# Optimization experiments

Hardware: AMD Instinct MI355X
Metric: run time of the kernel (lower is better)

The kernel has to match this reference:

```python
import jax, jax.numpy as jnp
import numpy as np

B, N, D = 8, 4096, 6          # clouds, points per cloud, coordinate dim
K = 64                        # max_num_neighbors in radius query
NS1, NS2 = 2048, 512          # fps ratios 0.5 and 0.25
R1, R2 = 0.2, 0.4             # ball-query radii
DIMS = {1: [6, 64, 64, 128], 2: [134, 128, 128, 256], 3: [262, 256, 512, 1024], 4: [1024, 512, 512]}


def setup_inputs():
    key = jax.random.key(0)
    k0, k1, k2 = jax.random.split(key, 3)
    inp = {}
    inp['synapse_cordi'] = jax.random.normal(k0, (B * N, D), jnp.float32)
    inp['batch_index'] = jnp.repeat(jnp.arange(B, dtype=jnp.int32), N)
    inp['weight'] = jax.random.uniform(k1, (B * N,), jnp.float32)
    k = k2
    for i, dims in DIMS.items():
        for j in range(len(dims) - 1):
            k, kw = jax.random.split(k)
            inp[f'w{i}_{j}'] = jax.random.normal(kw, (dims[j], dims[j + 1]), jnp.float32) * (1.0 / float(np.sqrt(dims[j])))
            inp[f'b{i}_{j}'] = jnp.zeros((dims[j + 1],), jnp.float32)
    return inp


def _mlp(x, params):
    # PyG MLP, plain_last=True; batch-norm at default (eval, running stats) is identity
    n = len(params)
    for i, (W, b) in enumerate(params):
        x = x @ W + b
        if i < n - 1:
            x = jax.nn.relu(x)
    return x


def _fps(pos, n_s):
    # farthest point sampling on one cloud [N, D] -> [n_s] indices (deterministic start at 0)
    d0 = jnp.sum((pos - pos[0]) ** 2, axis=-1)
    def step(mind, _):
        nxt = jnp.argmax(mind)
        mind = jnp.minimum(mind, jnp.sum((pos - pos[nxt]) ** 2, axis=-1))
        return mind, nxt
    _, idxs = jax.lax.scan(step, d0, None, length=n_s - 1)
    return jnp.concatenate([jnp.zeros((1,), idxs.dtype), idxs])


def _ball(pos, pos_q, r):
    # radius query: up to K nearest points within r for each query; [n_q,K] idx + validity mask
    d2 = jnp.sum((pos_q[:, None, :] - pos[None, :, :]) ** 2, axis=-1)  # [n_q, N]
    neg = jnp.where(d2 <= r * r, -d2, -jnp.inf)
    vals, nbr = jax.lax.top_k(neg, K)
    return nbr, vals > -jnp.inf


def _sa(x, pos, params, n_s, r):
    # Weight_Sample_Module: fps -> radius -> PointNetConv (gather, MLP, masked max-scatter)
    idx = jax.vmap(lambda p: _fps(p, n_s))(pos)                     # [B, n_s]
    pos_q = jnp.take_along_axis(pos, idx[..., None], axis=1)        # [B, n_s, D]
    nbr, valid = jax.vmap(lambda p, q: _ball(p, q, r))(pos, pos_q)  # [B, n_s, K]
    gather = lambda a: jax.vmap(lambda t, i: t[i])(a, nbr)          # [B, n_s, K, C]
    rel = gather(pos) - pos_q[:, :, None, :]
    feat = rel if x is None else jnp.concatenate([gather(x), rel], axis=-1)
    h = _mlp(feat, params)                                          # [B, n_s, K, C_out]
    h = jnp.where(valid[..., None], h, -jnp.inf)
    return jnp.max(h, axis=2), pos_q                                # max aggregation


def reference(synapse_cordi, batch_index, weight,
              w1_0, b1_0, w1_1, b1_1, w1_2, b1_2,
              w2_0, b2_0, w2_1, b2_1, w2_2, b2_2,
              w3_0, b3_0, w3_1, b3_1, w3_2, b3_2,
              w4_0, b4_0, w4_1, b4_1):
    pos = synapse_cordi.reshape(B, N, D)  # uniform clouds; batch_index = repeat(arange(B), N)
    p1 = [(w1_0, b1_0), (w1_1, b1_1), (w1_2, b1_2)]
    p2 = [(w2_0, b2_0), (w2_1, b2_1), (w2_2, b2_2)]
    p3 = [(w3_0, b3_0), (w3_1, b3_1), (w3_2, b3_2)]
    p4 = [(w4_0, b4_0), (w4_1, b4_1)]
    x1, pos1 = _sa(None, pos, p1, NS1, R1)   # [B, 2048, 128]
    x2, pos2 = _sa(x1, pos1, p2, NS2, R2)    # [B, 512, 256]
    h = _mlp(jnp.concatenate([x2, pos2], axis=-1), p3)  # [B, 512, 1024]
    g = jnp.max(h, axis=1)                   # global max pool -> [B, 1024]
    return _mlp(g, p4)                       # [B, 512]
```

## Files before the change

kernel.cpp:

```cpp
#include <hip/hip_runtime.h>
#include <math.h>

#define B_ 8
#define N_ 4096
#define D_ 6
#define K_ 64
#define NS1_ 2048
#define NS2_ 512

typedef float v2f __attribute__((ext_vector_type(2)));


__device__ __forceinline__ float dist2_rn(const float* __restrict__ a, const float* __restrict__ q) {
    float s = 0.f;
#pragma unroll
    for (int d = 0; d < 6; ++d) {
        float diff = __fsub_rn(a[d], q[d]);
        s = __fadd_rn(s, __fmul_rn(diff, diff));
    }
    return s;
}

__device__ __forceinline__ unsigned mapf(float x) {
    unsigned u = __float_as_uint(x);
    return (u & 0x80000000u) ? ~u : (u | 0x80000000u);
}
__device__ __forceinline__ float unmapf(unsigned u) {
    return __uint_as_float((u & 0x80000000u) ? (u & 0x7FFFFFFFu) : ~u);
}

template <int CTRL>
__device__ __forceinline__ double dppd(double k) {
    int lo = __double2loint(k), hi = __double2hiint(k);
    int nlo = __builtin_amdgcn_update_dpp(lo, lo, CTRL, 0xF, 0xF, false);
    int nhi = __builtin_amdgcn_update_dpp(hi, hi, CTRL, 0xF, 0xF, false);
    return __hiloint2double(nhi, nlo);
}


__device__ __forceinline__ void wait_flag(unsigned* f, int t) {
    if (t == 0) {
        while (__hip_atomic_load(f, __ATOMIC_RELAXED, __HIP_MEMORY_SCOPE_AGENT) == 0u)
            __builtin_amdgcn_s_sleep(32);
        __builtin_amdgcn_fence(__ATOMIC_ACQUIRE, "agent");
    }
    __syncthreads();
}


template <int NP, int NS>
__device__ __forceinline__ void fps_core(float* __restrict__ spos, int* __restrict__ sidx,
                                         double* __restrict__ part, int t) {
#pragma clang fp contract(off)
    constexpr int NT = 256;
    constexpr int P = NP / NT;
    constexpr int HP = P / 2;
    int lane = t & 63, w = t >> 6;

    v2f px2[HP][6];
#pragma unroll
    for (int j = 0; j < HP; ++j)
#pragma unroll
        for (int d = 0; d < 6; ++d) {
            px2[j][d].x = spos[(t + NT * (2 * j)) * 6 + d];
            px2[j][d].y = spos[(t + NT * (2 * j + 1)) * 6 + d];
        }

    float cx[6];
#pragma unroll
    for (int d = 0; d < 6; ++d) cx[d] = spos[d];

    v2f mind2[HP];
    float runv = -1.f;
    int runj = 0;
#pragma unroll
    for (int j = 0; j < HP; ++j) {
        v2f d2 = {0.f, 0.f};
#pragma unroll
        for (int d = 0; d < 6; ++d) {
            v2f df = px2[j][d] - cx[d];
            d2 = d2 + df * df;
        }
        mind2[j] = d2;
        if (d2.x > runv) { runv = d2.x; runj = t + NT * (2 * j); }
        if (d2.y > runv) { runv = d2.y; runj = t + NT * (2 * j + 1); }
    }

    for (int s = 1; s < NS; ++s) {
        double key = __hiloint2double((int)__float_as_uint(runv), (int)(unsigned)(~runj));
        key = fmax(key, dppd<0x111>(key));
        key = fmax(key, dppd<0x112>(key));
        key = fmax(key, dppd<0x114>(key));
        key = fmax(key, dppd<0x118>(key));
        key = fmax(key, dppd<0x142>(key));
        key = fmax(key, dppd<0x143>(key));
        if (lane == 63) part[(s & 1) * 4 + w] = key;
        __syncthreads();
        double kk = part[(s & 1) * 4 + (lane & 3)];
        kk = fmax(kk, dppd<0x111>(kk));
        kk = fmax(kk, dppd<0x112>(kk));
        int nx = ~__builtin_amdgcn_readlane(__double2loint(kk), 3);
        if (t == 0) sidx[s] = nx;

        const float2* sv2 = (const float2*)spos;
        float2 ca = sv2[nx * 3], cb = sv2[nx * 3 + 1], cc = sv2[nx * 3 + 2];
        cx[0] = ca.x; cx[1] = ca.y; cx[2] = cb.x; cx[3] = cb.y; cx[4] = cc.x; cx[5] = cc.y;

        runv = -1.f;
        runj = 0;
#pragma unroll
        for (int j = 0; j < HP; ++j) {
            v2f d2 = {0.f, 0.f};
#pragma unroll
            for (int d = 0; d < 6; ++d) {
                v2f df = px2[j][d] - cx[d];
                d2 = d2 + df * df;
            }
            float mx = fminf(mind2[j].x, d2.x);
            float my = fminf(mind2[j].y, d2.y);
            mind2[j].x = mx;
            mind2[j].y = my;
            if (mx > runv) { runv = mx; runj = t + NT * (2 * j); }
            if (my > runv) { runv = my; runj = t + NT * (2 * j + 1); }
        }
    }
}


template <int NPTS, int S>
__device__ __forceinline__ void ball_scan(const float* __restrict__ sp,
                                          const float* __restrict__ posq,
                                          int* __restrict__ nbr, int* __restrict__ cnt,
                                          float r2, int qid, int tid,
                                          float* __restrict__ sd, unsigned short* __restrict__ si) {
    float q[6];
#pragma unroll
    for (int d = 0; d < 6; ++d) q[d] = posq[(size_t)qid * 6 + d];

    int n = 0;
    float thr = INFINITY;
#pragma unroll 4
    for (int j = 0; j < NPTS; ++j) {
        float d2 = dist2_rn(sp + j * 6, q);
        if (d2 <= r2 && (n < K_ || d2 < thr)) {
            int i = (n < K_) ? n : (K_ - 1);
            if (n < K_) ++n;
            while (i > 0 && sd[(i - 1) * S + tid] > d2) {
                sd[i * S + tid] = sd[(i - 1) * S + tid];
                si[i * S + tid] = si[(i - 1) * S + tid];
                --i;
            }
            sd[i * S + tid] = d2;
            si[i * S + tid] = (unsigned short)j;
            if (n == K_) thr = sd[(K_ - 1) * S + tid];
        }
    }
    cnt[qid] = n;
    for (int i = 0; i < n; ++i) nbr[(size_t)qid * K_ + i] = (int)si[i * S + tid];
}


__global__ __launch_bounds__(256, 1) void stage12_kernel(
        const float* __restrict__ pos, float* __restrict__ pos1,
        int* __restrict__ nbr1, int* __restrict__ cnt1,
        float* __restrict__ pos2, int* __restrict__ nbr2, int* __restrict__ cnt2,
        unsigned* __restrict__ g, unsigned* flags,
        float r2_1, float r2_2) {
    __shared__ union Smem {
        struct { float spos[N_ * 6]; int sidx[NS1_]; double part[8]; } fps;
        struct { float spos[N_ * 6]; float sd[K_ * 128]; unsigned short si[K_ * 128]; } b1;
        struct { float spos[NS1_ * 6]; float sd[K_ * 64]; unsigned short si[K_ * 64]; } b2;
    } sm;
    int t = threadIdx.x;

    if (blockIdx.x < 8) {
        int b = blockIdx.x;
        float* spos = sm.fps.spos;
        int* sidx = sm.fps.sidx;
        double* part = sm.fps.part;

        {
            const float4* src = (const float4*)(pos + (size_t)b * N_ * 6);
            float4* dst = (float4*)spos;
            for (int e = t; e < N_ * 6 / 4; e += 256) dst[e] = src[e];
        }
        if (t == 0) sidx[0] = 0;
        __syncthreads();

        fps_core<N_, NS1_>(spos, sidx, part, t);
        __syncthreads();

        float smp[NS1_ / 256][6];
#pragma unroll
        for (int i = 0; i < NS1_ / 256; ++i) {
            int s = t + 256 * i;
            int ix = sidx[s];
#pragma unroll
            for (int d = 0; d < 6; ++d) smp[i][d] = spos[ix * 6 + d];
        }
#pragma unroll
        for (int i = 0; i < NS1_ / 256; ++i) {
            int s = t + 256 * i;
#pragma unroll
            for (int d = 0; d < 6; ++d) pos1[((size_t)b * NS1_ + s) * 6 + d] = smp[i][d];
        }
        __syncthreads();
        if (t == 0) {
            __threadfence();
            __hip_atomic_store(&flags[b], 1u, __ATOMIC_RELEASE, __HIP_MEMORY_SCOPE_AGENT);
        }

#pragma unroll
        for (int i = 0; i < NS1_ / 256; ++i) {
            int s = t + 256 * i;
#pragma unroll
            for (int d = 0; d < 6; ++d) spos[s * 6 + d] = smp[i][d];
        }
        for (int e = t; e < 1024; e += 256) g[b * 1024 + e] = 0u;
        if (t == 0) sidx[0] = 0;
        __syncthreads();

        fps_core<NS1_, NS2_>(spos, sidx, part, t);
        __syncthreads();

        for (int s = t; s < NS2_; s += 256) {
            int ix = sidx[s];
#pragma unroll
            for (int d = 0; d < 6; ++d) pos2[((size_t)b * NS2_ + s) * 6 + d] = spos[ix * 6 + d];
        }
        __syncthreads();
        if (t == 0) {
            __threadfence();
            __hip_atomic_store(&flags[8 + b], 1u, __ATOMIC_RELEASE, __HIP_MEMORY_SCOPE_AGENT);
        }
    } else if (blockIdx.x < 8 + 128) {
        int blk = blockIdx.x - 8;
        int b = blk >> 4;
        {
            const float4* src = (const float4*)(pos + (size_t)b * N_ * 6);
            float4* dst = (float4*)sm.b1.spos;
            for (int e = t; e < N_ * 6 / 4; e += 256) dst[e] = src[e];
        }
        __syncthreads();
        wait_flag(&flags[b], t);
        if (t < 128) {
            int qid = blk * 128 + t;
            ball_scan<N_, 128>(sm.b1.spos, pos1, nbr1, cnt1, r2_1, qid, t, sm.b1.sd, sm.b1.si);
        }
    } else {
        int blk = blockIdx.x - 136;
        int b = blk >> 3;
        wait_flag(&flags[b], t);
        {
            const float4* src = (const float4*)(pos1 + (size_t)b * NS1_ * 6);
            float4* dst = (float4*)sm.b2.spos;
            for (int e = t; e < NS1_ * 6 / 4; e += 256) dst[e] = src[e];
        }
        __syncthreads();
        wait_flag(&flags[8 + b], t);
        if (t < 64) {
            int qid = blk * 64 + t;
            ball_scan<NS1_, 64>(sm.b2.spos, pos2, nbr2, cnt2, r2_2, qid, t, sm.b2.sd, sm.b2.si);
        }
    }
}


__global__ __launch_bounds__(256) void sa1_kernel(const float* __restrict__ pos,
                                                  const float* __restrict__ pos1,
                                                  const int* __restrict__ nbr1,
                                                  const int* __restrict__ cnt1,
                                                  const float* __restrict__ W1, const float* __restrict__ B1,
                                                  const float* __restrict__ W2, const float* __restrict__ B2,
                                                  const float* __restrict__ W3, const float* __restrict__ B3,
                                                  float* __restrict__ x1) {
    int lane = threadIdx.x & 63;
    int w = threadIdx.x >> 6;
    int qid = blockIdx.x * 4 + w;
    int b = qid / NS1_;
    const float* p = pos + (size_t)b * N_ * 6;
    float q[6];
#pragma unroll
    for (int d = 0; d < 6; ++d) q[d] = pos1[(size_t)qid * 6 + d];
    int c = cnt1[qid];
    float m0 = -INFINITY, m1 = -INFINITY;

    for (int n = 0; n < c; ++n) {
        int j = nbr1[(size_t)qid * K_ + n];
        float rel[6];
#pragma unroll
        for (int d = 0; d < 6; ++d) rel[d] = p[(size_t)j * 6 + d] - q[d];
        float a = B1[lane];
#pragma unroll
        for (int d = 0; d < 6; ++d) a = fmaf(W1[d * 64 + lane], rel[d], a);
        float h1 = fmaxf(a, 0.f);
        float a2 = B2[lane];
        for (int k = 0; k < 64; ++k) {
            float v = __shfl(h1, k, 64);
            a2 = fmaf(W2[k * 64 + lane], v, a2);
        }
        float h2 = fmaxf(a2, 0.f);
        float o0 = B3[lane], o1 = B3[64 + lane];
        for (int k = 0; k < 64; ++k) {
            float v = __shfl(h2, k, 64);
            o0 = fmaf(W3[k * 128 + lane], v, o0);
            o1 = fmaf(W3[k * 128 + 64 + lane], v, o1);
        }
        m0 = fmaxf(m0, o0);
        m1 = fmaxf(m1, o1);
    }
    x1[(size_t)qid * 128 + lane] = m0;
    x1[(size_t)qid * 128 + 64 + lane] = m1;
}


__global__ __launch_bounds__(256) void sa2_conv(const float* __restrict__ pos1, const float* __restrict__ posq,
                                                const int* __restrict__ nbr, const int* __restrict__ cnt,
                                                const float* __restrict__ x1,
                                                const float* __restrict__ W1, const float* __restrict__ B1,
                                                const float* __restrict__ W2, const float* __restrict__ B2,
                                                const float* __restrict__ W3, const float* __restrict__ B3,
                                                float* __restrict__ out) {
    int lane = threadIdx.x & 63;
    int w = threadIdx.x >> 6;
    int qid = blockIdx.x * 4 + w;
    int b = qid / NS2_;
    float q[6];
#pragma unroll
    for (int d = 0; d < 6; ++d) q[d] = posq[(size_t)qid * 6 + d];
    int c = cnt[qid];
    float m0 = -INFINITY, m1 = -INFINITY, m2 = -INFINITY, m3 = -INFINITY;

    for (int n = 0; n < c; ++n) {
        int j = nbr[(size_t)qid * K_ + n];
        size_t row = (size_t)b * NS1_ + j;
        const float* xs = x1 + row * 128;
        float rel[6];
#pragma unroll
        for (int d = 0; d < 6; ++d) rel[d] = pos1[row * 6 + d] - q[d];
        float a0 = B1[lane], a1 = B1[64 + lane];
        for (int k = 0; k < 128; ++k) {
            float v = xs[k];
            a0 = fmaf(W1[k * 128 + lane], v, a0);
            a1 = fmaf(W1[k * 128 + 64 + lane], v, a1);
        }
#pragma unroll
        for (int d = 0; d < 6; ++d) {
            float v = rel[d];
            a0 = fmaf(W1[(128 + d) * 128 + lane], v, a0);
            a1 = fmaf(W1[(128 + d) * 128 + 64 + lane], v, a1);
        }
        float h1a = fmaxf(a0, 0.f), h1b = fmaxf(a1, 0.f);
        float c0 = B2[lane], c1 = B2[64 + lane];
        for (int k = 0; k < 64; ++k) {
            float v = __shfl(h1a, k, 64);
            c0 = fmaf(W2[k * 128 + lane], v, c0);
            c1 = fmaf(W2[k * 128 + 64 + lane], v, c1);
        }
        for (int k = 0; k < 64; ++k) {
            float v = __shfl(h1b, k, 64);
            c0 = fmaf(W2[(64 + k) * 128 + lane], v, c0);
            c1 = fmaf(W2[(64 + k) * 128 + 64 + lane], v, c1);
        }
        float h2a = fmaxf(c0, 0.f), h2b = fmaxf(c1, 0.f);
        float e0 = B3[lane], e1 = B3[64 + lane], e2 = B3[128 + lane], e3 = B3[192 + lane];
        for (int k = 0; k < 64; ++k) {
            float v = __shfl(h2a, k, 64);
            e0 = fmaf(W3[k * 256 + lane], v, e0);
            e1 = fmaf(W3[k * 256 + 64 + lane], v, e1);
            e2 = fmaf(W3[k * 256 + 128 + lane], v, e2);
            e3 = fmaf(W3[k * 256 + 192 + lane], v, e3);
        }
        for (int k = 0; k < 64; ++k) {
            float v = __shfl(h2b, k, 64);
            e0 = fmaf(W3[(64 + k) * 256 + lane], v, e0);
            e1 = fmaf(W3[(64 + k) * 256 + 64 + lane], v, e1);
            e2 = fmaf(W3[(64 + k) * 256 + 128 + lane], v, e2);
            e3 = fmaf(W3[(64 + k) * 256 + 192 + lane], v, e3);
        }
        m0 = fmaxf(m0, e0);
        m1 = fmaxf(m1, e1);
        m2 = fmaxf(m2, e2);
        m3 = fmaxf(m3, e3);
    }
    out[(size_t)qid * 256 + lane] = m0;
    out[(size_t)qid * 256 + 64 + lane] = m1;
    out[(size_t)qid * 256 + 128 + lane] = m2;
    out[(size_t)qid * 256 + 192 + lane] = m3;
}


__global__ __launch_bounds__(256, 1) void mlp3_kernel(const float* __restrict__ x2, const float* __restrict__ pos2,
                                                      const float* __restrict__ W0, const float* __restrict__ B0,
                                                      const float* __restrict__ W1, const float* __restrict__ B1,
                                                      const float* __restrict__ W2, const float* __restrict__ B2,
                                                      unsigned* __restrict__ g) {
    int lane = threadIdx.x & 63;
    int w = threadIdx.x >> 6;
    int qid0 = blockIdx.x * 16 + w * 4;
    int b = qid0 >> 9;

    float xr[4][4];
#pragma unroll
    for (int q = 0; q < 4; ++q)
#pragma unroll
        for (int j = 0; j < 4; ++j) xr[q][j] = x2[(size_t)(qid0 + q) * 256 + j * 64 + lane];

    float a[4][4];
    {
        float4 bv = *(const float4*)&B0[lane * 4];
#pragma unroll
        for (int q = 0; q < 4; ++q) { a[q][0] = bv.x; a[q][1] = bv.y; a[q][2] = bv.z; a[q][3] = bv.w; }
    }
#pragma unroll
    for (int j = 0; j < 4; ++j) {
        for (int k2 = 0; k2 < 64; ++k2) {
            int k = j * 64 + k2;
            float4 wv = *(const float4*)&W0[(size_t)k * 256 + lane * 4];
#pragma unroll
            for (int q = 0; q < 4; ++q) {
                float v = __shfl(xr[q][j], k2, 64);
                a[q][0] = fmaf(wv.x, v, a[q][0]);
                a[q][1] = fmaf(wv.y, v, a[q][1]);
                a[q][2] = fmaf(wv.z, v, a[q][2]);
                a[q][3] = fmaf(wv.w, v, a[q][3]);
            }
        }
    }
#pragma unroll
    for (int d = 0; d < 6; ++d) {
        float4 wv = *(const float4*)&W0[(size_t)(256 + d) * 256 + lane * 4];
#pragma unroll
        for (int q = 0; q < 4; ++q) {
            float v = pos2[(size_t)(qid0 + q) * 6 + d];
            a[q][0] = fmaf(wv.x, v, a[q][0]);
            a[q][1] = fmaf(wv.y, v, a[q][1]);
            a[q][2] = fmaf(wv.z, v, a[q][2]);
            a[q][3] = fmaf(wv.w, v, a[q][3]);
        }
    }
    float h1[4][4];
#pragma unroll
    for (int q = 0; q < 4; ++q)
#pragma unroll
        for (int u = 0; u < 4; ++u) h1[q][u] = fmaxf(a[q][u], 0.f);

    float c[4][8];
    {
        float4 b0 = *(const float4*)&B1[lane * 8];
        float4 b1 = *(const float4*)&B1[lane * 8 + 4];
#pragma unroll
        for (int q = 0; q < 4; ++q) {
            c[q][0] = b0.x; c[q][1] = b0.y; c[q][2] = b0.z; c[q][3] = b0.w;
            c[q][4] = b1.x; c[q][5] = b1.y; c[q][6] = b1.z; c[q][7] = b1.w;
        }
    }
    for (int l = 0; l < 64; ++l) {
#pragma unroll
        for (int r = 0; r < 4; ++r) {
            int k = l * 4 + r;
            float4 w0 = *(const float4*)&W1[(size_t)k * 512 + lane * 8];
            float4 w1 = *(const float4*)&W1[(size_t)k * 512 + lane * 8 + 4];
#pragma unroll
            for (int q = 0; q < 4; ++q) {
                float v = __shfl(h1[q][r], l, 64);
                c[q][0] = fmaf(w0.x, v, c[q][0]);
                c[q][1] = fmaf(w0.y, v, c[q][1]);
                c[q][2] = fmaf(w0.z, v, c[q][2]);
                c[q][3] = fmaf(w0.w, v, c[q][3]);
                c[q][4] = fmaf(w1.x, v, c[q][4]);
                c[q][5] = fmaf(w1.y, v, c[q][5]);
                c[q][6] = fmaf(w1.z, v, c[q][6]);
                c[q][7] = fmaf(w1.w, v, c[q][7]);
            }
        }
    }
    float h2[4][8];
#pragma unroll
    for (int q = 0; q < 4; ++q)
#pragma unroll
        for (int u = 0; u < 8; ++u) h2[q][u] = fmaxf(c[q][u], 0.f);

    float e[4][16];
#pragma unroll
    for (int jj = 0; jj < 4; ++jj) {
        float4 bv = *(const float4*)&B2[lane * 16 + jj * 4];
#pragma unroll
        for (int q = 0; q < 4; ++q) {
            e[q][jj * 4 + 0] = bv.x; e[q][jj * 4 + 1] = bv.y;
            e[q][jj * 4 + 2] = bv.z; e[q][jj * 4 + 3] = bv.w;
        }
    }
    for (int l = 0; l < 64; ++l) {
#pragma unroll
        for (int r = 0; r < 8; ++r) {
            int k = l * 8 + r;
            const float* wp = &W2[(size_t)k * 1024 + lane * 16];
            float4 w0 = *(const float4*)&wp[0];
            float4 w1 = *(const float4*)&wp[4];
            float4 w2 = *(const float4*)&wp[8];
            float4 w3 = *(const float4*)&wp[12];
#pragma unroll
            for (int q = 0; q < 4; ++q) {
                float v = __shfl(h2[q][r], l, 64);
                e[q][0]  = fmaf(w0.x, v, e[q][0]);
                e[q][1]  = fmaf(w0.y, v, e[q][1]);
                e[q][2]  = fmaf(w0.z, v, e[q][2]);
                e[q][3]  = fmaf(w0.w, v, e[q][3]);
                e[q][4]  = fmaf(w1.x, v, e[q][4]);
                e[q][5]  = fmaf(w1.y, v, e[q][5]);
                e[q][6]  = fmaf(w1.z, v, e[q][6]);
                e[q][7]  = fmaf(w1.w, v, e[q][7]);
                e[q][8]  = fmaf(w2.x, v, e[q][8]);
                e[q][9]  = fmaf(w2.y, v, e[q][9]);
                e[q][10] = fmaf(w2.z, v, e[q][10]);
                e[q][11] = fmaf(w2.w, v, e[q][11]);
                e[q][12] = fmaf(w3.x, v, e[q][12]);
                e[q][13] = fmaf(w3.y, v, e[q][13]);
                e[q][14] = fmaf(w3.z, v, e[q][14]);
                e[q][15] = fmaf(w3.w, v, e[q][15]);
            }
        }
    }
#pragma unroll
    for (int u = 0; u < 16; ++u) {
        float m = fmaxf(fmaxf(e[0][u], e[1][u]), fmaxf(e[2][u], e[3][u]));
        atomicMax(&g[b * 1024 + lane * 16 + u], mapf(m));
    }
}


__global__ __launch_bounds__(512) void mlp4_kernel(const unsigned* __restrict__ g,
                                                   const float* __restrict__ W0, const float* __restrict__ B0,
                                                   const float* __restrict__ W1, const float* __restrict__ B1,
                                                   float* __restrict__ out) {
    int b = blockIdx.x;
    int c = threadIdx.x;
    __shared__ float h[512];
    float a = B0[c];
    for (int k = 0; k < 1024; ++k) {
        float v = unmapf(g[b * 1024 + k]);
        a = fmaf(v, W0[k * 512 + c], a);
    }
    h[c] = fmaxf(a, 0.f);
    __syncthreads();
    float o = B1[c];
    for (int k = 0; k < 512; ++k) o = fmaf(h[k], W1[k * 512 + c], o);
    out[(size_t)b * 512 + c] = o;
}


extern "C" void kernel_launch(void* const* d_in, const int* in_sizes, int n_in,
                              void* d_out, int out_size, void* d_ws, size_t ws_size,
                              hipStream_t stream) {
    const float* pos = (const float*)d_in[0];
    const float* w1_0 = (const float*)d_in[3];
    const float* b1_0 = (const float*)d_in[4];
    const float* w1_1 = (const float*)d_in[5];
    const float* b1_1 = (const float*)d_in[6];
    const float* w1_2 = (const float*)d_in[7];
    const float* b1_2 = (const float*)d_in[8];
    const float* w2_0 = (const float*)d_in[9];
    const float* b2_0 = (const float*)d_in[10];
    const float* w2_1 = (const float*)d_in[11];
    const float* b2_1 = (const float*)d_in[12];
    const float* w2_2 = (const float*)d_in[13];
    const float* b2_2 = (const float*)d_in[14];
    const float* w3_0 = (const float*)d_in[15];
    const float* b3_0 = (const float*)d_in[16];
    const float* w3_1 = (const float*)d_in[17];
    const float* b3_1 = (const float*)d_in[18];
    const float* w3_2 = (const float*)d_in[19];
    const float* b3_2 = (const float*)d_in[20];
    const float* w4_0 = (const float*)d_in[21];
    const float* b4_0 = (const float*)d_in[22];
    const float* w4_1 = (const float*)d_in[23];
    const float* b4_1 = (const float*)d_in[24];
    float* out = (float*)d_out;

    char* ws = (char*)d_ws;
    size_t off = 0;
    float* pos1 = (float*)(ws + off);  off += (size_t)B_ * NS1_ * 6 * 4;
    int* nbr1 = (int*)(ws + off);      off += (size_t)B_ * NS1_ * K_ * 4;
    int* cnt1 = (int*)(ws + off);      off += (size_t)B_ * NS1_ * 4;
    float* x1 = (float*)(ws + off);    off += (size_t)B_ * NS1_ * 128 * 4;
    float* pos2 = (float*)(ws + off);  off += (size_t)B_ * NS2_ * 6 * 4;
    int* nbr2 = (int*)(ws + off);      off += (size_t)B_ * NS2_ * K_ * 4;
    int* cnt2 = (int*)(ws + off);      off += (size_t)B_ * NS2_ * 4;
    float* x2 = (float*)(ws + off);    off += (size_t)B_ * NS2_ * 256 * 4;
    unsigned* g = (unsigned*)(ws + off); off += (size_t)B_ * 1024 * 4;
    unsigned* flags = (unsigned*)(ws + off); off += 64;

    const float r2_1 = (float)(0.2 * 0.2);
    const float r2_2 = (float)(0.4 * 0.4);

    hipMemsetAsync(flags, 0, 64, stream);

    stage12_kernel<<<200, 256, 0, stream>>>(pos, pos1, nbr1, cnt1, pos2, nbr2, cnt2, g,
                                            flags, r2_1, r2_2);
    sa1_kernel<<<(B_ * NS1_) / 4, 256, 0, stream>>>(pos, pos1, nbr1, cnt1,
                                                    w1_0, b1_0, w1_1, b1_1, w1_2, b1_2, x1);
    sa2_conv<<<(B_ * NS2_) / 4, 256, 0, stream>>>(pos1, pos2, nbr2, cnt2, x1,
                                                  w2_0, b2_0, w2_1, b2_1, w2_2, b2_2, x2);
    mlp3_kernel<<<(B_ * NS2_) / 16, 256, 0, stream>>>(x2, pos2, w3_0, b3_0, w3_1, b3_1, w3_2, b3_2, g);
    mlp4_kernel<<<B_, 512, 0, stream>>>(g, w4_0, b4_0, w4_1, b4_1, out);
}
```

Before: 2.497 ms.

## Fuse ball query, SA1/SA2 convs and MLP3 into one persistent kernel

Folds the SA1 conv, SA2 conv and MLP3 global max-pool into the stage12 kernel. Each of 128 worker blocks runs its ball query and then immediately applies the MLP using the neighbor lists and point positions already in shared memory, so the nbr/cnt/x2 arrays are never written to global memory. A per-batch counter flag is added so SA2 can wait until every SA1 block of its cloud has finished, and the separate sa1/sa2/mlp3 launches are removed. The cost is that all the heavy MLP work now runs on only 128 blocks of 4 waves. That is far less parallelism than the thousands of blocks the separate kernels used, and the extra spin-waits can serialize further.

After: 2.770 ms. 10.9% more time.

```diff
diff --git a/kernel.cpp b/kernel.cpp
--- a/kernel.cpp
+++ b/kernel.cpp
@@ -42,6 +42,15 @@
     if (t == 0) {
         while (__hip_atomic_load(f, __ATOMIC_RELAXED, __HIP_MEMORY_SCOPE_AGENT) == 0u)
             __builtin_amdgcn_s_sleep(32);
+        __builtin_amdgcn_fence(__ATOMIC_ACQUIRE, "agent");
+    }
+    __syncthreads();
+}
+
+__device__ __forceinline__ void wait_count(unsigned* f, unsigned tgt, int t) {
+    if (t == 0) {
+        while (__hip_atomic_load(f, __ATOMIC_RELAXED, __HIP_MEMORY_SCOPE_AGENT) < tgt)
+            __builtin_amdgcn_s_sleep(8);
         __builtin_amdgcn_fence(__ATOMIC_ACQUIRE, "agent");
     }
     __syncthreads();
@@ -128,11 +137,10 @@
 
 
 template <int NPTS, int S>
-__device__ __forceinline__ void ball_scan(const float* __restrict__ sp,
-                                          const float* __restrict__ posq,
-                                          int* __restrict__ nbr, int* __restrict__ cnt,
-                                          float r2, int qid, int tid,
-                                          float* __restrict__ sd, unsigned short* __restrict__ si) {
+__device__ __forceinline__ int ball_scan(const float* __restrict__ sp,
+                                         const float* __restrict__ posq,
+                                         float r2, int qid, int tid,
+                                         float* __restrict__ sd, unsigned short* __restrict__ si) {
     float q[6];
 #pragma unroll
     for (int d = 0; d < 6; ++d) q[d] = posq[(size_t)qid * 6 + d];
@@ -155,23 +163,32 @@
             if (n == K_) thr = sd[(K_ - 1) * S + tid];
         }
     }
-    cnt[qid] = n;
-    for (int i = 0; i < n; ++i) nbr[(size_t)qid * K_ + i] = (int)si[i * S + tid];
+    return n;
 }
 
 
 __global__ __launch_bounds__(256, 1) void stage12_kernel(
-        const float* __restrict__ pos, float* __restrict__ pos1,
-        int* __restrict__ nbr1, int* __restrict__ cnt1,
-        float* __restrict__ pos2, int* __restrict__ nbr2, int* __restrict__ cnt2,
-        unsigned* __restrict__ g, unsigned* flags,
+        const float* __restrict__ pos, float* __restrict__ pos1, float* __restrict__ pos2,
+        float* __restrict__ x1, unsigned* __restrict__ g, unsigned* flags,
+        const float* __restrict__ W1_0, const float* __restrict__ B1_0,
+        const float* __restrict__ W1_1, const float* __restrict__ B1_1,
+        const float* __restrict__ W1_2, const float* __restrict__ B1_2,
+        const float* __restrict__ W2_0, const float* __restrict__ B2_0,
+        const float* __restrict__ W2_1, const float* __restrict__ B2_1,
+        const float* __restrict__ W2_2, const float* __restrict__ B2_2,
+        const float* __restrict__ W3_0, const float* __restrict__ B3_0,
+        const float* __restrict__ W3_1, const float* __restrict__ B3_1,
+        const float* __restrict__ W3_2, const float* __restrict__ B3_2,
         float r2_1, float r2_2) {
     __shared__ union Smem {
         struct { float spos[N_ * 6]; int sidx[NS1_]; double part[8]; } fps;
-        struct { float spos[N_ * 6]; float sd[K_ * 128]; unsigned short si[K_ * 128]; } b1;
-        struct { float spos[NS1_ * 6]; float sd[K_ * 64]; unsigned short si[K_ * 64]; } b2;
+        struct { float spos[N_ * 6]; float sd[K_ * 128]; unsigned short si[K_ * 128];
+                 unsigned short scnt[128]; } p1;
+        struct { float spos1[NS1_ * 6]; float sd2[K_ * 32]; unsigned short si2[K_ * 32];
+                 unsigned short scnt2[32]; float sx2[32 * 256]; } p2;
     } sm;
     int t = threadIdx.x;
+    int lane = t & 63, w = t >> 6;
 
     if (blockIdx.x < 8) {
         int b = blockIdx.x;
@@ -233,299 +250,281 @@
             __threadfence();
             __hip_atomic_store(&flags[8 + b], 1u, __ATOMIC_RELEASE, __HIP_MEMORY_SCOPE_AGENT);
         }
-    } else if (blockIdx.x < 8 + 128) {
-        int blk = blockIdx.x - 8;
-        int b = blk >> 4;
+        return;
+    }
+
+    int blk = blockIdx.x - 8;
+    int b = blk >> 4, sub = blk & 15;
+
+    {
+        const float4* src = (const float4*)(pos + (size_t)b * N_ * 6);
+        float4* dst = (float4*)sm.p1.spos;
+        for (int e = t; e < N_ * 6 / 4; e += 256) dst[e] = src[e];
+    }
+    __syncthreads();
+    wait_flag(&flags[b], t);
+
+    int qbase1 = b * NS1_ + sub * 128;
+    if (t < 128) {
+        int n = ball_scan<N_, 128>(sm.p1.spos, pos1, r2_1, qbase1 + t, t, sm.p1.sd, sm.p1.si);
+        sm.p1.scnt[t] = (unsigned short)n;
+    }
+    __syncthreads();
+
+    for (int qq = 0; qq < 32; ++qq) {
+        int lq = w * 32 + qq;
+        int qid = qbase1 + lq;
+        float q[6];
+#pragma unroll
+        for (int d = 0; d < 6; ++d) q[d] = pos1[(size_t)qid * 6 + d];
+        int c = sm.p1.scnt[lq];
+        float m0 = -INFINITY, m1 = -INFINITY;
+        for (int n = 0; n < c; ++n) {
+            int j = sm.p1.si[n * 128 + lq];
+            float rel[6];
+#pragma unroll
+            for (int d = 0; d < 6; ++d) rel[d] = sm.p1.spos[j * 6 + d] - q[d];
+            float a = B1_0[lane];
+#pragma unroll
+            for (int d = 0; d < 6; ++d) a = fmaf(W1_0[d * 64 + lane], rel[d], a);
+            float h1 = fmaxf(a, 0.f);
+            float a2 = B1_1[lane];
+            for (int k = 0; k < 64; ++k) {
+                float v = __shfl(h1, k, 64);
+                a2 = fmaf(W1_1[k * 64 + lane], v, a2);
+            }
+            float h2 = fmaxf(a2, 0.f);
+            float o0 = B1_2[lane], o1 = B1_2[64 + lane];
+            for (int k = 0; k < 64; ++k) {
+                float v = __shfl(h2, k, 64);
+                o0 = fmaf(W1_2[k * 128 + lane], v, o0);
+                o1 = fmaf(W1_2[k * 128 + 64 + lane], v, o1);
+            }
+            m0 = fmaxf(m0, o0);
+            m1 = fmaxf(m1, o1);
+        }
+        x1[(size_t)qid * 128 + lane] = m0;
+        x1[(size_t)qid * 128 + 64 + lane] = m1;
+    }
+    __syncthreads();
+    if (t == 0) {
+        __threadfence();
+        __hip_atomic_fetch_add(&flags[16 + b], 1u, __ATOMIC_RELEASE, __HIP_MEMORY_SCOPE_AGENT);
+    }
+
+    {
+        const float4* src = (const float4*)(pos1 + (size_t)b * NS1_ * 6);
+        float4* dst = (float4*)sm.p2.spos1;
+        for (int e = t; e < NS1_ * 6 / 4; e += 256) dst[e] = src[e];
+    }
+    __syncthreads();
+    wait_flag(&flags[8 + b], t);
+
+    int qbase2 = b * NS2_ + sub * 32;
+    if (t < 32) {
+        int n = ball_scan<NS1_, 32>(sm.p2.spos1, pos2, r2_2, qbase2 + t, t, sm.p2.sd2, sm.p2.si2);
+        sm.p2.scnt2[t] = (unsigned short)n;
+    }
+    __syncthreads();
+    wait_count(&flags[16 + b], 16u, t);
+
+    for (int qq = 0; qq < 8; ++qq) {
+        int lq = w * 8 + qq;
+        int qid = qbase2 + lq;
+        float q[6];
+#pragma unroll
+        for (int d = 0; d < 6; ++d) q[d] = pos2[(size_t)qid * 6 + d];
+        int c = sm.p2.scnt2[lq];
+        float m0 = -INFINITY, m1 = -INFINITY, m2 = -INFINITY, m3 = -INFINITY;
+        for (int n = 0; n < c; ++n) {
+            int j = sm.p2.si2[n * 32 + lq];
+            const float* xs = x1 + ((size_t)b * NS1_ + j) * 128;
+            float rel[6];
+#pragma unroll
+            for (int d = 0; d < 6; ++d) rel[d] = sm.p2.spos1[j * 6 + d] - q[d];
+            float a0 = B2_0[lane], a1 = B2_0[64 + lane];
+            for (int k = 0; k < 128; ++k) {
+                float v = xs[k];
+                a0 = fmaf(W2_0[k * 128 + lane], v, a0);
+                a1 = fmaf(W2_0[k * 128 + 64 + lane], v, a1);
+            }
+#pragma unroll
+            for (int d = 0; d < 6; ++d) {
+                float v = rel[d];
+                a0 = fmaf(W2_0[(128 + d) * 128 + lane], v, a0);
+                a1 = fmaf(W2_0[(128 + d) * 128 + 64 + lane], v, a1);
+            }
+            float h1a = fmaxf(a0, 0.f), h1b = fmaxf(a1, 0.f);
+            float c0 = B2_1[lane], c1 = B2_1[64 + lane];
+            for (int k = 0; k < 64; ++k) {
+                float v = __shfl(h1a, k, 64);
+                c0 = fmaf(W2_1[k * 128 + lane], v, c0);
+                c1 = fmaf(W2_1[k * 128 + 64 + lane], v, c1);
+            }
+            for (int k = 0; k < 64; ++k) {
+                float v = __shfl(h1b, k, 64);
+                c0 = fmaf(W2_1[(64 + k) * 128 + lane], v, c0);
+                c1 = fmaf(W2_1[(64 + k) * 128 + 64 + lane], v, c1);
+            }
+            float h2a = fmaxf(c0, 0.f), h2b = fmaxf(c1, 0.f);
+            float e0 = B2_2[lane], e1 = B2_2[64 + lane], e2 = B2_2[128 + lane], e3 = B2_2[192 + lane];
+            for (int k = 0; k < 64; ++k) {
+                float v = __shfl(h2a, k, 64);
+                e0 = fmaf(W2_2[k * 256 + lane], v, e0);
+                e1 = fmaf(W2_2[k * 256 + 64 + lane], v, e1);
+                e2 = fmaf(W2_2[k * 256 + 128 + lane], v, e2);
+                e3 = fmaf(W2_2[k * 256 + 192 + lane], v, e3);
+            }
+            for (int k = 0; k < 64; ++k) {
+                float v = __shfl(h2b, k, 64);
+                e0 = fmaf(W2_2[(64 + k) * 256 + lane], v, e0);
+                e1 = fmaf(W2_2[(64 + k) * 256 + 64 + lane], v, e1);
+                e2 = fmaf(W2_2[(64 + k) * 256 + 128 + lane], v, e2);
+                e3 = fmaf(W2_2[(64 + k) * 256 + 192 + lane], v, e3);
+            }
+            m0 = fmaxf(m0, e0);
+            m1 = fmaxf(m1, e1);
+            m2 = fmaxf(m2, e2);
+            m3 = fmaxf(m3, e3);
+        }
+        sm.p2.sx2[lq * 256 + lane] = m0;
+        sm.p2.sx2[lq * 256 + 64 + lane] = m1;
+        sm.p2.sx2[lq * 256 + 128 + lane] = m2;
+        sm.p2.sx2[lq * 256 + 192 + lane] = m3;
+    }
+    __syncthreads();
+
+    for (int pass = 0; pass < 2; ++pass) {
+        int lq0 = w * 8 + pass * 4;
+        int qid0 = qbase2 + lq0;
+
+        float xr[4][4];
+#pragma unroll
+        for (int q = 0; q < 4; ++q)
+#pragma unroll
+            for (int j = 0; j < 4; ++j) xr[q][j] = sm.p2.sx2[(lq0 + q) * 256 + j * 64 + lane];
+
+        float a[4][4];
         {
-            const float4* src = (const float4*)(pos + (size_t)b * N_ * 6);
-            float4* dst = (float4*)sm.b1.spos;
-            for (int e = t; e < N_ * 6 / 4; e += 256) dst[e] = src[e];
-        }
-        __syncthreads();
-        wait_flag(&flags[b], t);
-        if (t < 128) {
-            int qid = blk * 128 + t;
-            ball_scan<N_, 128>(sm.b1.spos, pos1, nbr1, cnt1, r2_1, qid, t, sm.b1.sd, sm.b1.si);
-        }
-    } else {
-        int blk = blockIdx.x - 136;
-        int b = blk >> 3;
-        wait_flag(&flags[b], t);
-        {
-            const float4* src = (const float4*)(pos1 + (size_t)b * NS1_ * 6);
-            float4* dst = (float4*)sm.b2.spos;
-            for (int e = t; e < NS1_ * 6 / 4; e += 256) dst[e] = src[e];
-        }
-        __syncthreads();
-        wait_flag(&flags[8 + b], t);
-        if (t < 64) {
-            int qid = blk * 64 + t;
-            ball_scan<NS1_, 64>(sm.b2.spos, pos2, nbr2, cnt2, r2_2, qid, t, sm.b2.sd, sm.b2.si);
-        }
-    }
-}
-
-
-__global__ __launch_bounds__(256) void sa1_kernel(const float* __restrict__ pos,
-                                                  const float* __restrict__ pos1,
-                                                  const int* __restrict__ nbr1,
-                                                  const int* __restrict__ cnt1,
-                                                  const float* __restrict__ W1, const float* __restrict__ B1,
-                                                  const float* __restrict__ W2, const float* __restrict__ B2,
-                                                  const float* __restrict__ W3, const float* __restrict__ B3,
-                                                  float* __restrict__ x1) {
-    int lane = threadIdx.x & 63;
-    int w = threadIdx.x >> 6;
-    int qid = blockIdx.x * 4 + w;
-    int b = qid / NS1_;
-    const float* p = pos + (size_t)b * N_ * 6;
-    float q[6];
-#pragma unroll
-    for (int d = 0; d < 6; ++d) q[d] = pos1[(size_t)qid * 6 + d];
-    int c = cnt1[qid];
-    float m0 = -INFINITY, m1 = -INFINITY;
-
-    for (int n = 0; n < c; ++n) {
-        int j = nbr1[(size_t)qid * K_ + n];
-        float rel[6];
-#pragma unroll
-        for (int d = 0; d < 6; ++d) rel[d] = p[(size_t)j * 6 + d] - q[d];
-        float a = B1[lane];
-#pragma unroll
-        for (int d = 0; d < 6; ++d) a = fmaf(W1[d * 64 + lane], rel[d], a);
-        float h1 = fmaxf(a, 0.f);
-        float a2 = B2[lane];
-        for (int k = 0; k < 64; ++k) {
-            float v = __shfl(h1, k, 64);
-            a2 = fmaf(W2[k * 64 + lane], v, a2);
-        }
-        float h2 = fmaxf(a2, 0.f);
-        float o0 = B3[lane], o1 = B3[64 + lane];
-        for (int k = 0; k < 64; ++k) {
-            float v = __shfl(h2, k, 64);
-            o0 = fmaf(W3[k * 128 + lane], v, o0);
-            o1 = fmaf(W3[k * 128 + 64 + lane], v, o1);
-        }
-        m0 = fmaxf(m0, o0);
-        m1 = fmaxf(m1, o1);
-    }
-    x1[(size_t)qid * 128 + lane] = m0;
-    x1[(size_t)qid * 128 + 64 + lane] = m1;
-}
-
-
-__global__ __launch_bounds__(256) void sa2_conv(const float* __restrict__ pos1, const float* __restrict__ posq,
-                                                const int* __restrict__ nbr, const int* __restrict__ cnt,
-                                                const float* __restrict__ x1,
-                                                const float* __restrict__ W1, const float* __restrict__ B1,
-                                                const float* __restrict__ W2, const float* __restrict__ B2,
-                                                const float* __restrict__ W3, const float* __restrict__ B3,
-                                                float* __restrict__ out) {
-    int lane = threadIdx.x & 63;
-    int w = threadIdx.x >> 6;
-    int qid = blockIdx.x * 4 + w;
-    int b = qid / NS2_;
-    float q[6];
-#pragma unroll
-    for (int d = 0; d < 6; ++d) q[d] = posq[(size_t)qid * 6 + d];
-    int c = cnt[qid];
-    float m0 = -INFINITY, m1 = -INFINITY, m2 = -INFINITY, m3 = -INFINITY;
-
-    for (int n = 0; n < c; ++n) {
-        int j = nbr[(size_t)qid * K_ + n];
-        size_t row = (size_t)b * NS1_ + j;
-        const float* xs = x1 + row * 128;
-        float rel[6];
-#pragma unroll
-        for (int d = 0; d < 6; ++d) rel[d] = pos1[row * 6 + d] - q[d];
-        float a0 = B1[lane], a1 = B1[64 + lane];
-        for (int k = 0; k < 128; ++k) {
-            float v = xs[k];
-            a0 = fmaf(W1[k * 128 + lane], v, a0);
-            a1 = fmaf(W1[k * 128 + 64 + lane], v, a1);
+            float4 bv = *(const float4*)&B3_0[lane * 4];
+#pragma unroll
+            for (int q = 0; q < 4; ++q) { a[q][0] = bv.x; a[q][1] = bv.y; a[q][2] = bv.z; a[q][3] = bv.w; }
+        }
+#pragma unroll
+        for (int j = 0; j < 4; ++j) {
+            for (int k2 = 0; k2 < 64; ++k2) {
+                int k = j * 64 + k2;
+                float4 wv = *(const float4*)&W3_0[(size_t)k * 256 + lane * 4];
+#pragma unroll
+                for (int q = 0; q < 4; ++q) {
+                    float v = __shfl(xr[q][j], k2, 64);
+                    a[q][0] = fmaf(wv.x, v, a[q][0]);
+                    a[q][1] = fmaf(wv.y, v, a[q][1]);
+                    a[q][2] = fmaf(wv.z, v, a[q][2]);
+                    a[q][3] = fmaf(wv.w, v, a[q][3]);
+                }
+            }
         }
 #pragma unroll
         for (int d = 0; d < 6; ++d) {
-            float v = rel[d];
-            a0 = fmaf(W1[(128 + d) * 128 + lane], v, a0);
-            a1 = fmaf(W1[(128 + d) * 128 + 64 + lane], v, a1);
-        }
-        float h1a = fmaxf(a0, 0.f), h1b = fmaxf(a1, 0.f);
-        float c0 = B2[lane], c1 = B2[64 + lane];
-        for (int k = 0; k < 64; ++k) {
-            float v = __shfl(h1a, k, 64);
-            c0 = fmaf(W2[k * 128 + lane], v, c0);
-            c1 = fmaf(W2[k * 128 + 64 + lane], v, c1);
-        }
-        for (int k = 0; k < 64; ++k) {
-            float v = __shfl(h1b, k, 64);
-            c0 = fmaf(W2[(64 + k) * 128 + lane], v, c0);
-            c1 = fmaf(W2[(64 + k) * 128 + 64 + lane], v, c1);
-        }
-        float h2a = fmaxf(c0, 0.f), h2b = fmaxf(c1, 0.f);
-        float e0 = B3[lane], e1 = B3[64 + lane], e2 = B3[128 + lane], e3 = B3[192 + lane];
-        for (int k = 0; k < 64; ++k) {
-            float v = __shfl(h2a, k, 64);
-            e0 = fmaf(W3[k * 256 + lane], v, e0);
-            e1 = fmaf(W3[k * 256 + 64 + lane], v, e1);
-            e2 = fmaf(W3[k * 256 + 128 + lane], v, e2);
-            e3 = fmaf(W3[k * 256 + 192 + lane], v, e3);
-        }
-        for (int k = 0; k < 64; ++k) {
-            float v = __shfl(h2b, k, 64);
-            e0 = fmaf(W3[(64 + k) * 256 + lane], v, e0);
-            e1 = fmaf(W3[(64 + k) * 256 + 64 + lane], v, e1);
-            e2 = fmaf(W3[(64 + k) * 256 + 128 + lane], v, e2);
-            e3 = fmaf(W3[(64 + k) * 256 + 192 + lane], v, e3);
-        }
-        m0 = fmaxf(m0, e0);
-        m1 = fmaxf(m1, e1);
-        m2 = fmaxf(m2, e2);
-        m3 = fmaxf(m3, e3);
-    }
-    out[(size_t)qid * 256 + lane] = m0;
-    out[(size_t)qid * 256 + 64 + lane] = m1;
-    out[(size_t)qid * 256 + 128 + lane] = m2;
-    out[(size_t)qid * 256 + 192 + lane] = m3;
-}
-
-
-__global__ __launch_bounds__(256, 1) void mlp3_kernel(const float* __restrict__ x2, const float* __restrict__ pos2,
-                                                      const float* __restrict__ W0, const float* __restrict__ B0,
-                                                      const float* __restrict__ W1, const float* __restrict__ B1,
-                                                      const float* __restrict__ W2, const float* __restrict__ B2,
-                                                      unsigned* __restrict__ g) {
-    int lane = threadIdx.x & 63;
-    int w = threadIdx.x >> 6;
-    int qid0 = blockIdx.x * 16 + w * 4;
-    int b = qid0 >> 9;
-
-    float xr[4][4];
-#pragma unroll
-    for (int q = 0; q < 4; ++q)
-#pragma unroll
-        for (int j = 0; j < 4; ++j) xr[q][j] = x2[(size_t)(qid0 + q) * 256 + j * 64 + lane];
-
-    float a[4][4];
-    {
-        float4 bv = *(const float4*)&B0[lane * 4];
-#pragma unroll
-        for (int q = 0; q < 4; ++q) { a[q][0] = bv.x; a[q][1] = bv.y; a[q][2] = bv.z; a[q][3] = bv.w; }
-    }
-#pragma unroll
-    for (int j = 0; j < 4; ++j) {
-        for (int k2 = 0; k2 < 64; ++k2) {
-            int k = j * 64 + k2;
-            float4 wv = *(const float4*)&W0[(size_t)k * 256 + lane * 4];
+            float4 wv = *(const float4*)&W3_0[(size_t)(256 + d) * 256 + lane * 4];
 #pragma unroll
             for (int q = 0; q < 4; ++q) {
-                float v = __shfl(xr[q][j], k2, 64);
+                float v = pos2[(size_t)(qid0 + q) * 6 + d];
                 a[q][0] = fmaf(wv.x, v, a[q][0]);
                 a[q][1] = fmaf(wv.y, v, a[q][1]);
                 a[q][2] = fmaf(wv.z, v, a[q][2]);
                 a[q][3] = fmaf(wv.w, v, a[q][3]);
             }
         }
-    }
-#pragma unroll
-    for (int d = 0; d < 6; ++d) {
-        float4 wv = *(const float4*)&W0[(size_t)(256 + d) * 256 + lane * 4];
-#pragma unroll
-        for (int q = 0; q < 4; ++q) {
-            float v = pos2[(size_t)(qid0 + q) * 6 + d];
-            a[q][0] = fmaf(wv.x, v, a[q][0]);
-            a[q][1] = fmaf(wv.y, v, a[q][1]);
-            a[q][2] = fmaf(wv.z, v, a[q][2]);
-            a[q][3] = fmaf(wv.w, v, a[q][3]);
-        }
-    }
-    float h1[4][4];
-#pragma unroll
-    for (int q = 0; q < 4; ++q)
-#pragma unroll
-        for (int u = 0; u < 4; ++u) h1[q][u] = fmaxf(a[q][u], 0.f);
-
-    float c[4][8];
-    {
-        float4 b0 = *(const float4*)&B1[lane * 8];
-        float4 b1 = *(const float4*)&B1[lane * 8 + 4];
-#pragma unroll
-        for (int q = 0; q < 4; ++q) {
-            c[q][0] = b0.x; c[q][1] = b0.y; c[q][2] = b0.z; c[q][3] = b0.w;
-            c[q][4] = b1.x; c[q][5] = b1.y; c[q][6] = b1.z; c[q][7] = b1.w;
-        }
-    }
-    for (int l = 0; l < 64; ++l) {
-#pragma unroll
-        for (int r = 0; r < 4; ++r) {
-            int k = l * 4 + r;
-            float4 w0 = *(const float4*)&W1[(size_t)k * 512 + lane * 8];
-            float4 w1 = *(const float4*)&W1[(size_t)k * 512 + lane * 8 + 4];
+        float h1[4][4];
+#pragma unroll
+        for (int q = 0; q < 4; ++q)
+#pragma unroll
+            for (int u = 0; u < 4; ++u) h1[q][u] = fmaxf(a[q][u], 0.f);
+
+        float c[4][8];
+        {
+            float4 b0 = *(const float4*)&B3_1[lane * 8];
+            float4 b1 = *(const float4*)&B3_1[lane * 8 + 4];
 #pragma unroll
             for (int q = 0; q < 4; ++q) {
-                float v = __shfl(h1[q][r], l, 64);
-                c[q][0] = fmaf(w0.x, v, c[q][0]);
-                c[q][1] = fmaf(w0.y, v, c[q][1]);
-                c[q][2] = fmaf(w0.z, v, c[q][2]);
-                c[q][3] = fmaf(w0.w, v, c[q][3]);
-                c[q][4] = fmaf(w1.x, v, c[q][4]);
-                c[q][5] = fmaf(w1.y, v, c[q][5]);
-                c[q][6] = fmaf(w1.z, v, c[q][6]);
-                c[q][7] = fmaf(w1.w, v, c[q][7]);
-            }
-        }
-    }
-    float h2[4][8];
-#pragma unroll
-    for (int q = 0; q < 4; ++q)
-#pragma unroll
-        for (int u = 0; u < 8; ++u) h2[q][u] = fmaxf(c[q][u], 0.f);
-
-    float e[4][16];
-#pragma unroll
-    for (int jj = 0; jj < 4; ++jj) {
-        float4 bv = *(const float4*)&B2[lane * 16 + jj * 4];
-#pragma unroll
-        for (int q = 0; q < 4; ++q) {
-            e[q][jj * 4 + 0] = bv.x; e[q][jj * 4 + 1] = bv.y;
-            e[q][jj * 4 + 2] = bv.z; e[q][jj * 4 + 3] = bv.w;
-        }
-    }
-    for (int l = 0; l < 64; ++l) {
-#pragma unroll
-        for (int r = 0; r < 8; ++r) {
-            int k = l * 8 + r;
-            const float* wp = &W2[(size_t)k * 1024 + lane * 16];
-            float4 w0 = *(const float4*)&wp[0];
-            float4 w1 = *(const float4*)&wp[4];
-            float4 w2 = *(const float4*)&wp[8];
-            float4 w3 = *(const float4*)&wp[12];
+                c[q][0] = b0.x; c[q][1] = b0.y; c[q][2] = b0.z; c[q][3] = b0.w;
+                c[q][4] = b1.x; c[q][5] = b1.y; c[q][6] = b1.z; c[q][7] = b1.w;
+            }
+        }
+        for (int l = 0; l < 64; ++l) {
+#pragma unroll
+            for (int r = 0; r < 4; ++r) {
+                int k = l * 4 + r;
+                float4 w0 = *(const float4*)&W3_1[(size_t)k * 512 + lane * 8];
+                float4 w1 = *(const float4*)&W3_1[(size_t)k * 512 + lane * 8 + 4];
+#pragma unroll
+                for (int q = 0; q < 4; ++q) {
+                    float v = __shfl(h1[q][r], l, 64);
+                    c[q][0] = fmaf(w0.x, v, c[q][0]);
+                    c[q][1] = fmaf(w0.y, v, c[q][1]);
+                    c[q][2] = fmaf(w0.z, v, c[q][2]);
+                    c[q][3] = fmaf(w0.w, v, c[q][3]);
+                    c[q][4] = fmaf(w1.x, v, c[q][4]);
+                    c[q][5] = fmaf(w1.y, v, c[q][5]);
+                    c[q][6] = fmaf(w1.z, v, c[q][6]);
+                    c[q][7] = fmaf(w1.w, v, c[q][7]);
+                }
+            }
+        }
+        float h2[4][8];
+#pragma unroll
+        for (int q = 0; q < 4; ++q)
+#pragma unroll
+            for (int u = 0; u < 8; ++u) h2[q][u] = fmaxf(c[q][u], 0.f);
+
+        float e[4][16];
+#pragma unroll
+        for (int jj = 0; jj < 4; ++jj) {
+            float4 bv = *(const float4*)&B3_2[lane * 16 + jj * 4];
 #pragma unroll
             for (int q = 0; q < 4; ++q) {
-                float v = __shfl(h2[q][r], l, 64);
-                e[q][0]  = fmaf(w0.x, v, e[q][0]);
-                e[q][1]  = fmaf(w0.y, v, e[q][1]);
-                e[q][2]  = fmaf(w0.z, v, e[q][2]);
-                e[q][3]  = fmaf(w0.w, v, e[q][3]);
-                e[q][4]  = fmaf(w1.x, v, e[q][4]);
-                e[q][5]  = fmaf(w1.y, v, e[q][5]);
-                e[q][6]  = fmaf(w1.z, v, e[q][6]);
-                e[q][7]  = fmaf(w1.w, v, e[q][7]);
-                e[q][8]  = fmaf(w2.x, v, e[q][8]);
-                e[q][9]  = fmaf(w2.y, v, e[q][9]);
-                e[q][10] = fmaf(w2.z, v, e[q][10]);
-                e[q][11] = fmaf(w2.w, v, e[q][11]);
-                e[q][12] = fmaf(w3.x, v, e[q][12]);
-                e[q][13] = fmaf(w3.y, v, e[q][13]);
-                e[q][14] = fmaf(w3.z, v, e[q][14]);
-                e[q][15] = fmaf(w3.w, v, e[q][15]);
-            }
-        }
-    }
-#pragma unroll
-    for (int u = 0; u < 16; ++u) {
-        float m = fmaxf(fmaxf(e[0][u], e[1][u]), fmaxf(e[2][u], e[3][u]));
-        atomicMax(&g[b * 1024 + lane * 16 + u], mapf(m));
+                e[q][jj * 4 + 0] = bv.x; e[q][jj * 4 + 1] = bv.y;
+                e[q][jj * 4 + 2] = bv.z; e[q][jj * 4 + 3] = bv.w;
+            }
+        }
+        for (int l = 0; l < 64; ++l) {
+#pragma unroll
+            for (int r = 0; r < 8; ++r) {
+                int k = l * 8 + r;
+                const float* wp = &W3_2[(size_t)k * 1024 + lane * 16];
+                float4 w0 = *(const float4*)&wp[0];
+                float4 w1 = *(const float4*)&wp[4];
+                float4 w2 = *(const float4*)&wp[8];
+                float4 w3 = *(const float4*)&wp[12];
+#pragma unroll
+                for (int q = 0; q < 4; ++q) {
+                    float v = __shfl(h2[q][r], l, 64);
+                    e[q][0]  = fmaf(w0.x, v, e[q][0]);
+                    e[q][1]  = fmaf(w0.y, v, e[q][1]);
+                    e[q][2]  = fmaf(w0.z, v, e[q][2]);
+                    e[q][3]  = fmaf(w0.w, v, e[q][3]);
+                    e[q][4]  = fmaf(w1.x, v, e[q][4]);
+                    e[q][5]  = fmaf(w1.y, v, e[q][5]);
+                    e[q][6]  = fmaf(w1.z, v, e[q][6]);
+                    e[q][7]  = fmaf(w1.w, v, e[q][7]);
+                    e[q][8]  = fmaf(w2.x, v, e[q][8]);
+                    e[q][9]  = fmaf(w2.y, v, e[q][9]);
+                    e[q][10] = fmaf(w2.z, v, e[q][10]);
+                    e[q][11] = fmaf(w2.w, v, e[q][11]);
+                    e[q][12] = fmaf(w3.x, v, e[q][12]);
+                    e[q][13] = fmaf(w3.y, v, e[q][13]);
+                    e[q][14] = fmaf(w3.z, v, e[q][14]);
+                    e[q][15] = fmaf(w3.w, v, e[q][15]);
+                }
+            }
+        }
+#pragma unroll
+        for (int u = 0; u < 16; ++u) {
+            float m = fmaxf(fmaxf(e[0][u], e[1][u]), fmaxf(e[2][u], e[3][u]));
+            atomicMax(&g[b * 1024 + lane * 16 + u], mapf(m));
+        }
     }
 }
 
@@ -580,28 +579,21 @@
 
     char* ws = (char*)d_ws;
     size_t off = 0;
-    float* pos1 = (float*)(ws + off);  off += (size_t)B_ * NS1_ * 6 * 4;
-    int* nbr1 = (int*)(ws + off);      off += (size_t)B_ * NS1_ * K_ * 4;
-    int* cnt1 = (int*)(ws + off);      off += (size_t)B_ * NS1_ * 4;
-    float* x1 = (float*)(ws + off);    off += (size_t)B_ * NS1_ * 128 * 4;
-    float* pos2 = (float*)(ws + off);  off += (size_t)B_ * NS2_ * 6 * 4;
-    int* nbr2 = (int*)(ws + off);      off += (size_t)B_ * NS2_ * K_ * 4;
-    int* cnt2 = (int*)(ws + off);      off += (size_t)B_ * NS2_ * 4;
-    float* x2 = (float*)(ws + off);    off += (size_t)B_ * NS2_ * 256 * 4;
+    float* pos1 = (float*)(ws + off);    off += (size_t)B_ * NS1_ * 6 * 4;
+    float* pos2 = (float*)(ws + off);    off += (size_t)B_ * NS2_ * 6 * 4;
+    float* x1 = (float*)(ws + off);      off += (size_t)B_ * NS1_ * 128 * 4;
     unsigned* g = (unsigned*)(ws + off); off += (size_t)B_ * 1024 * 4;
-    unsigned* flags = (unsigned*)(ws + off); off += 64;
+    unsigned* flags = (unsigned*)(ws + off); off += 32 * 4;
 
     const float r2_1 = (float)(0.2 * 0.2);
     const float r2_2 = (float)(0.4 * 0.4);
 
-    hipMemsetAsync(flags, 0, 64, stream);
-
-    stage12_kernel<<<200, 256, 0, stream>>>(pos, pos1, nbr1, cnt1, pos2, nbr2, cnt2, g,
-                                            flags, r2_1, r2_2);
-    sa1_kernel<<<(B_ * NS1_) / 4, 256, 0, stream>>>(pos, pos1, nbr1, cnt1,
-                                                    w1_0, b1_0, w1_1, b1_1, w1_2, b1_2, x1);
-    sa2_conv<<<(B_ * NS2_) / 4, 256, 0, stream>>>(pos1, pos2, nbr2, cnt2, x1,
-                                                  w2_0, b2_0, w2_1, b2_1, w2_2, b2_2, x2);
-    mlp3_kernel<<<(B_ * NS2_) / 16, 256, 0, stream>>>(x2, pos2, w3_0, b3_0, w3_1, b3_1, w3_2, b3_2, g);
+    hipMemsetAsync(flags, 0, 32 * 4, stream);
+
+    stage12_kernel<<<136, 256, 0, stream>>>(pos, pos1, pos2, x1, g, flags,
+                                            w1_0, b1_0, w1_1, b1_1, w1_2, b1_2,
+                                            w2_0, b2_0, w2_1, b2_1, w2_2, b2_2,
+                                            w3_0, b3_0, w3_1, b3_1, w3_2, b3_2,
+                                            r2_1, r2_2);
     mlp4_kernel<<<B_, 512, 0, stream>>>(g, w4_0, b4_0, w4_1, b4_1, out);
 }
```
